# Kernel optimization log

Hardware: AMD Instinct MI355X
Metric: run time of the kernel (lower is better)

Reference implementation:

```python
import jax, jax.numpy as jnp
import numpy as np

NUM_TRAIN = 256  # num_train_anchors
N, A, T = 8, 131072, 64


def _make_boxes(key, shape2):
    # shape2 = (..., 2) of (y, x); returns valid boxes (y1, x1, y2, x2) in [0, 1]
    k1, k2 = jax.random.split(key)
    c1 = jax.random.uniform(k1, shape2, dtype=jnp.float32)
    c2 = jax.random.uniform(k2, shape2, dtype=jnp.float32)
    lo = jnp.minimum(c1, c2)
    hi = jnp.maximum(c1, c2)
    return jnp.stack([lo[..., 0], lo[..., 1], hi[..., 0], hi[..., 1]], axis=-1)


def setup_inputs() -> dict:
    key = jax.random.key(0)
    ka, kt, kp, kn = jax.random.split(key, 4)
    return {
        "anchors": _make_boxes(ka, (N, A, 2)),
        "true_bboxes": _make_boxes(kt, (N, T, 2)),
        "rand_pos": jax.random.uniform(kp, (N, A), dtype=jnp.float32),
        "rand_neg": jax.random.uniform(kn, (N, A), dtype=jnp.float32),
    }


def _bbox_overlap(anchors, gt):
    # anchors [A,4], gt [T,4] -> IoU [A,T]
    ay1, ax1, ay2, ax2 = [anchors[:, i] for i in range(4)]
    gy1, gx1, gy2, gx2 = [gt[:, i] for i in range(4)]
    a_area = (ay2 - ay1) * (ax2 - ax1)                       # [A]
    g_area = (gy2 - gy1) * (gx2 - gx1)                       # [T]
    ih = jnp.clip(jnp.minimum(ay2[:, None], gy2[None, :]) - jnp.maximum(ay1[:, None], gy1[None, :]), 0.0)
    iw = jnp.clip(jnp.minimum(ax2[:, None], gx2[None, :]) - jnp.maximum(ax1[:, None], gx1[None, :]), 0.0)
    inter = ih * iw                                          # [A,T]
    union = a_area[:, None] + g_area[None, :] - inter
    return jnp.where(union > 0, inter / jnp.where(union > 0, union, 1.0), 0.0)


def _rank_of(scores):
    # rank[i] = position of element i in ascending sort of scores
    order = jnp.argsort(scores)
    return jnp.zeros(scores.shape[0], jnp.int32).at[order].set(jnp.arange(scores.shape[0], dtype=jnp.int32))


def _compute_bbox_deltas(anchors, gt):
    # standard (dy, dx, dh, dw) encoding with safe denominators
    ah = anchors[:, 2] - anchors[:, 0]
    aw = anchors[:, 3] - anchors[:, 1]
    acy = anchors[:, 0] + 0.5 * ah
    acx = anchors[:, 1] + 0.5 * aw
    gh = gt[:, 2] - gt[:, 0]
    gw = gt[:, 3] - gt[:, 1]
    gcy = gt[:, 0] + 0.5 * gh
    gcx = gt[:, 1] + 0.5 * gw
    ah_s = jnp.where(ah > 0, ah, 1.0)
    aw_s = jnp.where(aw > 0, aw, 1.0)
    gh_s = jnp.where(gh > 0, gh, 1.0)
    gw_s = jnp.where(gw > 0, gw, 1.0)
    return jnp.stack([(gcy - acy) / ah_s, (gcx - acx) / aw_s,
                      jnp.log(gh_s / ah_s), jnp.log(gw_s / aw_s)], axis=-1)


def _get_targets(anchors, gt, r_pos, r_neg):
    na = anchors.shape[0]
    # strip_out_of_bounds_anchors: zero out anchors falling outside [0,1]^2 (keeps static shape)
    inb = (anchors[:, 0] >= 0) & (anchors[:, 1] >= 0) & (anchors[:, 2] <= 1) & (anchors[:, 3] <= 1)
    anchors = jnp.where(inb[:, None], anchors, 0.0)

    overlaps = _bbox_overlap(anchors, gt)                    # [A,T]

    # --- class assignment ---
    iou_max_val = jnp.max(overlaps, axis=1)                  # [A]
    classes = jnp.full((na,), -1, jnp.int32)
    classes = jnp.where(iou_max_val < 0.3, 0, classes)
    iou_max_anchor = jnp.argmax(overlaps, axis=0)            # [T] best anchor per gt
    pos_anchor = jnp.zeros((na,), jnp.int32).at[iou_max_anchor].set(1)
    classes = jnp.where(pos_anchor > 0, 1, classes)
    classes = jnp.where(iou_max_val >= 0.7, 1, classes)

    # --- subsample positives to NUM_TRAIN//2 (uniform random subset) ---
    pos = classes > 0
    rank_p = _rank_of(jnp.where(pos, r_pos, jnp.inf))
    keep_pos = pos & (rank_p < NUM_TRAIN // 2)
    classes = jnp.where(pos & ~keep_pos, -1, classes)
    n_pos = jnp.sum(keep_pos.astype(jnp.int32))

    # --- subsample negatives to NUM_TRAIN - n_pos ---
    desired_neg = NUM_TRAIN - n_pos
    neg = classes == 0
    rank_n = _rank_of(jnp.where(neg, r_neg, jnp.inf))
    keep_neg = neg & (rank_n < desired_neg)
    classes = jnp.where(neg & ~keep_neg, -1, classes)

    # --- deltas for positive anchors ---
    best_gt = jnp.argmax(overlaps, axis=1)                   # [A]
    deltas = _compute_bbox_deltas(anchors, gt[best_gt])      # [A,4]
    deltas = jnp.where((classes > 0)[:, None], deltas, 0.0)
    return classes, deltas


def reference(anchors, true_bboxes, rand_pos, rand_neg):
    classes, deltas = jax.vmap(_get_targets)(anchors, true_bboxes, rand_pos, rand_neg)
    return classes, deltas
```

## Files before the change

kernel.cpp:

```cpp
#include <hip/hip_runtime.h>
#include <stdint.h>

#define N_B 8
#define A_N 131072
#define T_N 64
#define NUM_TRAIN 256
#define NEG_TAU 0.05f
#define ITEM_CAP 1024
#define APT 4
#define GBLK 128
#define SEG 1024

typedef unsigned long long u64;
typedef unsigned int u32;

__device__ __forceinline__ float iou_one(float ay1, float ax1, float ay2, float ax2,
                                         float a_area, float gy1, float gx1, float gy2,
                                         float gx2, float g_area) {
#pragma clang fp contract(off)
    float ih = fmaxf(fminf(ay2, gy2) - fmaxf(ay1, gy1), 0.0f);
    float iw = fmaxf(fminf(ax2, gx2) - fmaxf(ax1, gx1), 0.0f);
    float inter = ih * iw;
    float uni = (a_area + g_area) - inter;
    return uni > 0.0f ? inter / uni : 0.0f;
}

__global__ void __launch_bounds__(256, 4) k_main(const float4* __restrict__ anchors4,
                                                 const float4* __restrict__ gts4,
                                                 const float* __restrict__ rpos,
                                                 const float* __restrict__ rneg,
                                                 unsigned char* __restrict__ preclass,
                                                 u64* __restrict__ colpart,
                                                 u64* __restrict__ pos_list,
                                                 u64* __restrict__ neg_list,
                                                 int* __restrict__ bcp, int* __restrict__ bcn) {
    __shared__ float4 gbox[T_N];
    __shared__ float gars[T_N];
    __shared__ u64 cmax[T_N];
    __shared__ int lp, ln;
    int n = blockIdx.y, bx = blockIdx.x, tid = threadIdx.x, lane = tid & 63;
    int a0 = bx * SEG + tid;
    size_t nA = (size_t)n * A_N;

    if (tid < T_N) {
        float4 gb = gts4[n * T_N + tid];
        gbox[tid] = gb;
        {
#pragma clang fp contract(off)
            gars[tid] = (gb.z - gb.x) * (gb.w - gb.y);
        }
        cmax[tid] = 0;
    }
    if (tid == 0) { lp = 0; ln = 0; }
    __syncthreads();

    float ay1[APT], ax1[APT], ay2[APT], ax2[APT], aar[APT], vmax[APT];
#pragma unroll
    for (int k = 0; k < APT; k++) {
        float4 ab = anchors4[nA + a0 + k * 256];
        float y1 = ab.x, x1 = ab.y, y2 = ab.z, x2 = ab.w;
        bool inb = (y1 >= 0.f) && (x1 >= 0.f) && (y2 <= 1.f) && (x2 <= 1.f);
        if (!inb) { y1 = x1 = y2 = x2 = 0.f; }
        ay1[k] = y1; ax1[k] = x1; ay2[k] = y2; ax2[k] = x2;
        {
#pragma clang fp contract(off)
            aar[k] = (y2 - y1) * (x2 - x1);
        }
        vmax[k] = 0.f;
    }

#pragma unroll 4
    for (int jj = 0; jj < T_N; jj++) {
        int j = (lane + jj) & (T_N - 1);
        float4 gb = gbox[j];
        float gar = gars[j];
        float vb = iou_one(ay1[0], ax1[0], ay2[0], ax2[0], aar[0], gb.x, gb.y, gb.z, gb.w, gar);
        vmax[0] = fmaxf(vmax[0], vb);
        int kb = 0;
#pragma unroll
        for (int k = 1; k < APT; k++) {
            float v = iou_one(ay1[k], ax1[k], ay2[k], ax2[k], aar[k], gb.x, gb.y, gb.z, gb.w, gar);
            vmax[k] = fmaxf(vmax[k], v);
            if (v > vb) { vb = v; kb = k; }
        }
        u64 pk = ((u64)__float_as_uint(vb) << 32) | (u32)(~(u32)(a0 + (kb << 8)));
        atomicMax(&cmax[j], pk);
    }

    size_t segbase = ((size_t)(n * GBLK + bx)) << 10;
#pragma unroll
    for (int k = 0; k < APT; k++) {
        int a = a0 + k * 256;
        float vm = vmax[k];
        int c0 = (vm < 0.3f) ? 0 : ((vm >= 0.7f) ? 1 : -1);
        preclass[nA + a] = (unsigned char)(signed char)c0;
        if (c0 == 1) {
            int s = atomicAdd(&lp, 1);
            pos_list[segbase + s] = ((u64)__float_as_uint(rpos[nA + a]) << 32) | (u32)a;
        } else if (c0 == 0) {
            float r = rneg[nA + a];
            if (r < NEG_TAU) {
                int s = atomicAdd(&ln, 1);
                neg_list[segbase + s] = ((u64)__float_as_uint(r) << 32) | (u32)a;
            }
        }
    }
    __syncthreads();
    if (tid < T_N) colpart[(size_t)((n << 6) + tid) * GBLK + bx] = cmax[tid];
    if (tid == 0) { bcp[n * GBLK + bx] = lp; bcn[n * GBLK + bx] = ln; }
}

__device__ u64 select_kth2(const u64* lists, const int* scnt,
                           const u64* extras, int ecnt, const u32* exbm,
                           int k, float scale, u64 ovf_all,
                           int* hist, u64* items, int* misc, int* wsum, u64* result) {
    int tid = threadIdx.x, lane = tid & 63, wid = tid >> 6;
    hist[tid] = 0;
    if (tid == 0) { misc[0] = 0; *result = ovf_all; }
    __syncthreads();

    int seg = tid >> 1, half = tid & 1;
    int c = scnt[seg];
    const ulonglong2* b2 = (const ulonglong2*)(lists + ((size_t)seg << 10));
    int nch = (c + 1) >> 1;

    {
        ulonglong2 q;
        if (half < nch) q = b2[half];
        for (int ci = half; ci < nch; ci += 2) {
            ulonglong2 qn;
            if (ci + 2 < nch) qn = b2[ci + 2];
            {
                u64 p = q.x; int a = (int)(u32)p;
                if (!exbm || !((exbm[a >> 5] >> (a & 31)) & 1)) {
                    float v = __uint_as_float((u32)(p >> 32));
                    int bb = (int)(v * scale); bb = bb > 255 ? 255 : bb;
                    atomicAdd(&hist[bb], 1);
                }
            }
            if (2 * ci + 1 < c) {
                u64 p = q.y; int a = (int)(u32)p;
                if (!exbm || !((exbm[a >> 5] >> (a & 31)) & 1)) {
                    float v = __uint_as_float((u32)(p >> 32));
                    int bb = (int)(v * scale); bb = bb > 255 ? 255 : bb;
                    atomicAdd(&hist[bb], 1);
                }
            }
            q = qn;
        }
    }
    for (int i = tid; i < ecnt; i += 256) {
        float v = __uint_as_float((u32)(extras[i] >> 32));
        int bb = (int)(v * scale); bb = bb > 255 ? 255 : bb;
        atomicAdd(&hist[bb], 1);
    }
    __syncthreads();

    int h = hist[tid], v = h;
#pragma unroll
    for (int d = 1; d < 64; d <<= 1) {
        int t = __shfl_up(v, d, 64);
        if (lane >= d) v += t;
    }
    if (lane == 63) wsum[wid] = v;
    __syncthreads();
    int base = 0;
    for (int w = 0; w < wid; w++) base += wsum[w];
    int total = wsum[0] + wsum[1] + wsum[2] + wsum[3];
    int incl = base + v, exc = incl - h;
    if (k >= exc && k < incl) { misc[1] = tid; misc[2] = exc; }
    __syncthreads();
    if (k >= total) return ovf_all;
    int b = misc[1], before = misc[2];

    {
        ulonglong2 q;
        if (half < nch) q = b2[half];
        for (int ci = half; ci < nch; ci += 2) {
            ulonglong2 qn;
            if (ci + 2 < nch) qn = b2[ci + 2];
            {
                u64 p = q.x; int a = (int)(u32)p;
                if (!exbm || !((exbm[a >> 5] >> (a & 31)) & 1)) {
                    float vv = __uint_as_float((u32)(p >> 32));
                    int bn = (int)(vv * scale); bn = bn > 255 ? 255 : bn;
                    if (bn == b) { int ix = atomicAdd(&misc[0], 1); if (ix < ITEM_CAP) items[ix] = p; }
                }
            }
            if (2 * ci + 1 < c) {
                u64 p = q.y; int a = (int)(u32)p;
                if (!exbm || !((exbm[a >> 5] >> (a & 31)) & 1)) {
                    float vv = __uint_as_float((u32)(p >> 32));
                    int bn = (int)(vv * scale); bn = bn > 255 ? 255 : bn;
                    if (bn == b) { int ix = atomicAdd(&misc[0], 1); if (ix < ITEM_CAP) items[ix] = p; }
                }
            }
            q = qn;
        }
    }
    for (int i = tid; i < ecnt; i += 256) {
        u64 p = extras[i];
        float vv = __uint_as_float((u32)(p >> 32));
        int bn = (int)(vv * scale); bn = bn > 255 ? 255 : bn;
        if (bn == b) { int ix = atomicAdd(&misc[0], 1); if (ix < ITEM_CAP) items[ix] = p; }
    }
    __syncthreads();
    int m = misc[0]; m = m < ITEM_CAP ? m : ITEM_CAP;
    int target = k - before;
    for (int i = tid; i < m; i += 256) {
        u64 p = items[i];
        int r = 0;
        for (int j = 0; j < m; j++) r += (items[j] < p);
        if (r == target) *result = p;
    }
    __syncthreads();
    u64 res = *result;
    __syncthreads();
    return res;
}

__global__ void __launch_bounds__(256) k_select(const u64* __restrict__ pos_list,
                                                const u64* __restrict__ neg_list,
                                                const int* __restrict__ bcp,
                                                const int* __restrict__ bcn,
                                                const u64* __restrict__ colpart,
                                                const unsigned char* __restrict__ preclass,
                                                const float* __restrict__ rpos,
                                                int* __restrict__ wnr_g,
                                                u64* __restrict__ cutoff) {
    __shared__ int sbp[GBLK], sbn[GBLK];
    __shared__ u64 cq[256];
    __shared__ int wnrs[T_N];
    __shared__ u64 extras[T_N];
    __shared__ int hist[256];
    __shared__ u64 items[ITEM_CAP];
    __shared__ u32 exbm[A_N / 32];
    __shared__ int misc[4];
    __shared__ u64 result;
    __shared__ int wsum[4];
    __shared__ int shr[9];
    int n = blockIdx.x, tid = threadIdx.x, lane = tid & 63, wid = tid >> 6;

    int pv = tid < GBLK ? bcp[n * GBLK + tid] : 0;
    int nv = tid < GBLK ? bcn[n * GBLK + tid] : 0;
    if (tid < GBLK) { sbp[tid] = pv; sbn[tid] = nv; }
#pragma unroll
    for (int off = 32; off > 0; off >>= 1) {
        pv += __shfl_xor(pv, off, 64);
        nv += __shfl_xor(nv, off, 64);
    }
    if (lane == 0) { shr[wid] = pv; shr[4 + wid] = nv; }

#pragma unroll
    for (int i = 0; i < A_N / 32 / 256; i++) exbm[tid + i * 256] = 0;

    {
        int t = tid >> 2, q = tid & 3;
        const u64* cp = colpart + (size_t)((n << 6) + t) * GBLK + q * 32;
        u64 m = 0;
#pragma unroll 8
        for (int i = 0; i < 32; i++) { u64 x = cp[i]; m = x > m ? x : m; }
        cq[tid] = m;
    }
    __syncthreads();
    if (tid < T_N) {
        u64 m = cq[tid * 4];
        u64 x = cq[tid * 4 + 1]; m = x > m ? x : m;
        x = cq[tid * 4 + 2]; m = x > m ? x : m;
        x = cq[tid * 4 + 3]; m = x > m ? x : m;
        int w = (int)(~(u32)(m & 0xFFFFFFFFull));
        wnrs[tid] = w;
        wnr_g[n * T_N + tid] = w;
        atomicOr(&exbm[w >> 5], 1u << (w & 31));
    }
    __syncthreads();
    if (tid < T_N) {
        int w = wnrs[tid];
        bool dup = false;
        for (int t2 = 0; t2 < tid; t2++) dup |= (wnrs[t2] == w);
        int pc = (int)(signed char)preclass[(size_t)n * A_N + w];
        bool val = !dup && (pc != 1);
        u64 mask = __ballot(val);
        if (val) {
            int ix = (int)__popcll(mask & ((1ull << lane) - 1));
            extras[ix] = ((u64)__float_as_uint(rpos[(size_t)n * A_N + w]) << 32) | (u32)w;
        }
        if (tid == 0) shr[8] = (int)__popcll(mask);
    }
    __syncthreads();
    int extra_cnt = shr[8];
    int P = shr[0] + shr[1] + shr[2] + shr[3] + extra_cnt;

    u64 cpos = select_kth2(pos_list + (((size_t)n * GBLK) << 10), sbp,
                           extras, extra_cnt, nullptr,
                           NUM_TRAIN / 2, 256.0f, ~0ull,
                           hist, items, misc, wsum, &result);
    int n_pos = P < NUM_TRAIN / 2 ? P : NUM_TRAIN / 2;
    int k_neg = NUM_TRAIN - n_pos;
    u64 cneg = select_kth2(neg_list + (((size_t)n * GBLK) << 10), sbn,
                           nullptr, 0, exbm,
                           k_neg, 256.0f / NEG_TAU, ((u64)__float_as_uint(NEG_TAU) << 32),
                           hist, items, misc, wsum, &result);
    if (tid == 0) { cutoff[2 * n] = cpos; cutoff[2 * n + 1] = cneg; }
}

__global__ void __launch_bounds__(256) k_final(const float4* __restrict__ anchors4,
                                               const float4* __restrict__ gts4,
                                               const u32* __restrict__ preclass32,
                                               const int* __restrict__ wnr_g,
                                               const float4* __restrict__ rpos4,
                                               const float4* __restrict__ rneg4,
                                               const u64* __restrict__ cutoff,
                                               float4* __restrict__ out_classes4,
                                               float4* __restrict__ out_deltas) {
    __shared__ float4 gbox[T_N];
    __shared__ float gars[T_N];
    __shared__ u32 wbm[32];
    int n = blockIdx.y, bx = blockIdx.x, tid = threadIdx.x;
    if (tid < 32) wbm[tid] = 0;
    __syncthreads();
    if (tid < T_N) {
        float4 gb = gts4[n * T_N + tid];
        gbox[tid] = gb;
        {
#pragma clang fp contract(off)
            gars[tid] = (gb.z - gb.x) * (gb.w - gb.y);
        }
        int w = wnr_g[n * T_N + tid];
        int d = w - bx * SEG;
        if ((u32)d < (u32)SEG) atomicOr(&wbm[d >> 5], 1u << (d & 31));
    }
    __syncthreads();

    size_t gi4 = ((size_t)n * A_N) / 4 + bx * 256 + tid;
    u32 pcw = preclass32[gi4];
    float4 rp = rpos4[gi4];
    float4 rn = rneg4[gi4];
    float rpv[4] = {rp.x, rp.y, rp.z, rp.w};
    float rnv[4] = {rn.x, rn.y, rn.z, rn.w};
    int a0 = (bx * 256 + tid) * 4;
    u64 cp = cutoff[2 * n], cn = cutoff[2 * n + 1];

    u32 marked = (wbm[tid >> 3] >> ((tid & 7) * 4)) & 0xF;

    float fcv[4];
#pragma unroll
    for (int j = 0; j < 4; j++) {
        int c = (int)(signed char)((pcw >> (8 * j)) & 0xFF);
        if ((marked >> j) & 1) c = 1;
        int a = a0 + j;
        int fc = -1;
        if (c == 1) {
            u64 p = ((u64)__float_as_uint(rpv[j]) << 32) | (u32)a;
            fc = (p < cp) ? 1 : -1;
        } else if (c == 0) {
            u64 p = ((u64)__float_as_uint(rnv[j]) << 32) | (u32)a;
            fc = (p < cn) ? 0 : -1;
        }
        fcv[j] = (float)fc;

        float4 d = make_float4(0.f, 0.f, 0.f, 0.f);
        if (fc == 1) {
            float4 ab = anchors4[(size_t)n * A_N + a];
            float ay1 = ab.x, ax1 = ab.y, ay2 = ab.z, ax2 = ab.w;
            bool inb = (ay1 >= 0.f) && (ax1 >= 0.f) && (ay2 <= 1.f) && (ax2 <= 1.f);
            if (!inb) { ay1 = ax1 = ay2 = ax2 = 0.f; }
            float a_area;
            {
#pragma clang fp contract(off)
                a_area = (ay2 - ay1) * (ax2 - ax1);
            }
            float vm = 0.f; int jb = 0;
            for (int t = 0; t < T_N; t++) {
                float4 gb = gbox[t];
                float v = iou_one(ay1, ax1, ay2, ax2, a_area, gb.x, gb.y, gb.z, gb.w, gars[t]);
                bool g = v > vm;
                vm = g ? v : vm;
                jb = g ? t : jb;
            }
            float4 gb = gbox[jb];
            float ah = ay2 - ay1, aw = ax2 - ax1;
            float acy = ay1 + 0.5f * ah, acx = ax1 + 0.5f * aw;
            float gh = gb.z - gb.x, gw = gb.w - gb.y;
            float gcy = gb.x + 0.5f * gh, gcx = gb.y + 0.5f * gw;
            float ah_s = ah > 0.f ? ah : 1.f, aw_s = aw > 0.f ? aw : 1.f;
            float gh_s = gh > 0.f ? gh : 1.f, gw_s = gw > 0.f ? gw : 1.f;
            d.x = (gcy - acy) / ah_s;
            d.y = (gcx - acx) / aw_s;
            d.z = logf(gh_s / ah_s);
            d.w = logf(gw_s / aw_s);
        }
        out_deltas[(size_t)n * A_N + a] = d;
    }
    out_classes4[gi4] = make_float4(fcv[0], fcv[1], fcv[2], fcv[3]);
}

extern "C" void kernel_launch(void* const* d_in, const int* in_sizes, int n_in,
                              void* d_out, int out_size, void* d_ws, size_t ws_size,
                              hipStream_t stream) {
    const float* anchors = (const float*)d_in[0];
    const float* gts     = (const float*)d_in[1];
    const float* rpos    = (const float*)d_in[2];
    const float* rneg    = (const float*)d_in[3];

    char* p = (char*)d_ws;
    u64* cutoff   = (u64*)p;  p += 2 * N_B * sizeof(u64);
    u64* colpart  = (u64*)p;  p += (size_t)N_B * T_N * GBLK * sizeof(u64);
    u64* pos_list = (u64*)p;  p += (size_t)N_B * GBLK * SEG * sizeof(u64);
    u64* neg_list = (u64*)p;  p += (size_t)N_B * GBLK * SEG * sizeof(u64);
    unsigned char* preclass = (unsigned char*)p; p += (size_t)N_B * A_N;
    int* bcp  = (int*)p;  p += N_B * GBLK * sizeof(int);
    int* bcn  = (int*)p;  p += N_B * GBLK * sizeof(int);
    int* wnr  = (int*)p;  p += N_B * T_N * sizeof(int);

    float* out_classes = (float*)d_out;
    float4* out_deltas = (float4*)(out_classes + (size_t)N_B * A_N);

    k_main<<<dim3(GBLK, N_B), 256, 0, stream>>>(
        (const float4*)anchors, (const float4*)gts, rpos, rneg,
        preclass, colpart, pos_list, neg_list, bcp, bcn);
    k_select<<<N_B, 256, 0, stream>>>(pos_list, neg_list, bcp, bcn, colpart,
                                      preclass, rpos, wnr, cutoff);
    k_final<<<dim3(GBLK, N_B), 256, 0, stream>>>(
        (const float4*)anchors, (const float4*)gts, (const u32*)preclass, wnr,
        (const float4*)rpos, (const float4*)rneg, cutoff,
        (float4*)out_classes, out_deltas);
}
```

Before: 176.4 us.

## Fuse three kernels into one cooperative kernel with grid syncs

Merges the main IoU pass, the selection and the final output pass into one cooperative kernel that separates the phases with grid.sync, and falls back to three launches when co-residency is not possible. The selection phase is split across two blocks per image, one for the positive cutoff and one for the negative cutoff. The large exclusion bitmap in shared memory is replaced by a small open-addressing hash set so the shared union stays small enough for full occupancy. This aims to remove launch gaps and serialized selection time, at the cost of grid-sync overhead and hash probing.

```diff
diff --git a/kernel.cpp b/kernel.cpp
--- a/kernel.cpp
+++ b/kernel.cpp
@@ -1,18 +1,29 @@
 #include <hip/hip_runtime.h>
+#include <hip/hip_cooperative_groups.h>
 #include <stdint.h>
+
+namespace cg = cooperative_groups;
 
 #define N_B 8
 #define A_N 131072
 #define T_N 64
 #define NUM_TRAIN 256
 #define NEG_TAU 0.05f
-#define ITEM_CAP 1024
+#define ITEM_CAP 512
+#define HSET 512
 #define APT 4
 #define GBLK 128
 #define SEG 1024
 
 typedef unsigned long long u64;
 typedef unsigned int u32;
+
+struct SA { float4 gbox[T_N]; float gars[T_N]; u64 cmax[T_N]; int lcnt[2]; };
+struct SB { int sbp[GBLK]; int sbn[GBLK]; u64 cq[256]; int wnrs[T_N]; u64 extras[T_N];
+            int hist[256]; u64 items[ITEM_CAP]; int hset[HSET];
+            int misc[4]; int wsum[4]; int shr[10]; u64 result; };
+struct SC { float4 gbox[T_N]; float gars[T_N]; u32 wbm[32]; };
+union SMem { SA a; SB b; SC c; };
 
 __device__ __forceinline__ float iou_one(float ay1, float ax1, float ay2, float ax2,
                                          float a_area, float gy1, float gx1, float gy2,
@@ -25,33 +36,36 @@
     return uni > 0.0f ? inter / uni : 0.0f;
 }
 
-__global__ void __launch_bounds__(256, 4) k_main(const float4* __restrict__ anchors4,
-                                                 const float4* __restrict__ gts4,
-                                                 const float* __restrict__ rpos,
-                                                 const float* __restrict__ rneg,
-                                                 unsigned char* __restrict__ preclass,
-                                                 u64* __restrict__ colpart,
-                                                 u64* __restrict__ pos_list,
-                                                 u64* __restrict__ neg_list,
-                                                 int* __restrict__ bcp, int* __restrict__ bcn) {
-    __shared__ float4 gbox[T_N];
-    __shared__ float gars[T_N];
-    __shared__ u64 cmax[T_N];
-    __shared__ int lp, ln;
-    int n = blockIdx.y, bx = blockIdx.x, tid = threadIdx.x, lane = tid & 63;
+__device__ __forceinline__ bool in_hset(const int* hset, int a) {
+    u32 h = ((u32)a * 2654435761u) >> 23 & (HSET - 1);
+    while (true) {
+        int v = hset[h];
+        if (v == -1) return false;
+        if (v == a) return true;
+        h = (h + 1) & (HSET - 1);
+    }
+}
+
+__device__ void phaseA(int n, int bx, const float4* __restrict__ anchors4,
+                       const float4* __restrict__ gts4, const float* __restrict__ rpos,
+                       const float* __restrict__ rneg, unsigned char* __restrict__ preclass,
+                       u64* __restrict__ colpart, u64* __restrict__ pos_list,
+                       u64* __restrict__ neg_list, int* __restrict__ bcp,
+                       int* __restrict__ bcn, SA* s) {
+    int tid = threadIdx.x, lane = tid & 63;
     int a0 = bx * SEG + tid;
     size_t nA = (size_t)n * A_N;
 
     if (tid < T_N) {
         float4 gb = gts4[n * T_N + tid];
-        gbox[tid] = gb;
+        s->gbox[tid] = gb;
         {
 #pragma clang fp contract(off)
-            gars[tid] = (gb.z - gb.x) * (gb.w - gb.y);
-        }
-        cmax[tid] = 0;
-    }
-    if (tid == 0) { lp = 0; ln = 0; }
+            s->gars[tid] = (gb.z - gb.x) * (gb.w - gb.y);
+        }
+        s->cmax[tid] = 0;
+    }
+    if (tid < 2) s->lcnt[tid] = 0;
     __syncthreads();
 
     float ay1[APT], ax1[APT], ay2[APT], ax2[APT], aar[APT], vmax[APT];
@@ -72,8 +86,8 @@
 #pragma unroll 4
     for (int jj = 0; jj < T_N; jj++) {
         int j = (lane + jj) & (T_N - 1);
-        float4 gb = gbox[j];
-        float gar = gars[j];
+        float4 gb = s->gbox[j];
+        float gar = s->gars[j];
         float vb = iou_one(ay1[0], ax1[0], ay2[0], ax2[0], aar[0], gb.x, gb.y, gb.z, gb.w, gar);
         vmax[0] = fmaxf(vmax[0], vb);
         int kb = 0;
@@ -84,7 +98,7 @@
             if (v > vb) { vb = v; kb = k; }
         }
         u64 pk = ((u64)__float_as_uint(vb) << 32) | (u32)(~(u32)(a0 + (kb << 8)));
-        atomicMax(&cmax[j], pk);
+        atomicMax(&s->cmax[j], pk);
     }
 
     size_t segbase = ((size_t)(n * GBLK + bx)) << 10;
@@ -95,28 +109,27 @@
         int c0 = (vm < 0.3f) ? 0 : ((vm >= 0.7f) ? 1 : -1);
         preclass[nA + a] = (unsigned char)(signed char)c0;
         if (c0 == 1) {
-            int s = atomicAdd(&lp, 1);
-            pos_list[segbase + s] = ((u64)__float_as_uint(rpos[nA + a]) << 32) | (u32)a;
+            int sl = atomicAdd(&s->lcnt[0], 1);
+            pos_list[segbase + sl] = ((u64)__float_as_uint(rpos[nA + a]) << 32) | (u32)a;
         } else if (c0 == 0) {
             float r = rneg[nA + a];
             if (r < NEG_TAU) {
-                int s = atomicAdd(&ln, 1);
-                neg_list[segbase + s] = ((u64)__float_as_uint(r) << 32) | (u32)a;
-            }
-        }
-    }
-    __syncthreads();
-    if (tid < T_N) colpart[(size_t)((n << 6) + tid) * GBLK + bx] = cmax[tid];
-    if (tid == 0) { bcp[n * GBLK + bx] = lp; bcn[n * GBLK + bx] = ln; }
+                int sl = atomicAdd(&s->lcnt[1], 1);
+                neg_list[segbase + sl] = ((u64)__float_as_uint(r) << 32) | (u32)a;
+            }
+        }
+    }
+    __syncthreads();
+    if (tid < T_N) colpart[(size_t)((n << 6) + tid) * GBLK + bx] = s->cmax[tid];
+    if (tid == 0) { bcp[n * GBLK + bx] = s->lcnt[0]; bcn[n * GBLK + bx] = s->lcnt[1]; }
 }
 
 __device__ u64 select_kth2(const u64* lists, const int* scnt,
-                           const u64* extras, int ecnt, const u32* exbm,
-                           int k, float scale, u64 ovf_all,
-                           int* hist, u64* items, int* misc, int* wsum, u64* result) {
+                           const u64* extras, int ecnt, bool use_excl,
+                           int k, float scale, u64 ovf_all, SB* s) {
     int tid = threadIdx.x, lane = tid & 63, wid = tid >> 6;
-    hist[tid] = 0;
-    if (tid == 0) { misc[0] = 0; *result = ovf_all; }
+    s->hist[tid] = 0;
+    if (tid == 0) { s->misc[0] = 0; s->result = ovf_all; }
     __syncthreads();
 
     int seg = tid >> 1, half = tid & 1;
@@ -132,18 +145,18 @@
             if (ci + 2 < nch) qn = b2[ci + 2];
             {
                 u64 p = q.x; int a = (int)(u32)p;
-                if (!exbm || !((exbm[a >> 5] >> (a & 31)) & 1)) {
+                if (!use_excl || !in_hset(s->hset, a)) {
                     float v = __uint_as_float((u32)(p >> 32));
                     int bb = (int)(v * scale); bb = bb > 255 ? 255 : bb;
-                    atomicAdd(&hist[bb], 1);
+                    atomicAdd(&s->hist[bb], 1);
                 }
             }
             if (2 * ci + 1 < c) {
                 u64 p = q.y; int a = (int)(u32)p;
-                if (!exbm || !((exbm[a >> 5] >> (a & 31)) & 1)) {
+                if (!use_excl || !in_hset(s->hset, a)) {
                     float v = __uint_as_float((u32)(p >> 32));
                     int bb = (int)(v * scale); bb = bb > 255 ? 255 : bb;
-                    atomicAdd(&hist[bb], 1);
+                    atomicAdd(&s->hist[bb], 1);
                 }
             }
             q = qn;
@@ -152,26 +165,26 @@
     for (int i = tid; i < ecnt; i += 256) {
         float v = __uint_as_float((u32)(extras[i] >> 32));
         int bb = (int)(v * scale); bb = bb > 255 ? 255 : bb;
-        atomicAdd(&hist[bb], 1);
-    }
-    __syncthreads();
-
-    int h = hist[tid], v = h;
+        atomicAdd(&s->hist[bb], 1);
+    }
+    __syncthreads();
+
+    int h = s->hist[tid], v = h;
 #pragma unroll
     for (int d = 1; d < 64; d <<= 1) {
         int t = __shfl_up(v, d, 64);
         if (lane >= d) v += t;
     }
-    if (lane == 63) wsum[wid] = v;
+    if (lane == 63) s->wsum[wid] = v;
     __syncthreads();
     int base = 0;
-    for (int w = 0; w < wid; w++) base += wsum[w];
-    int total = wsum[0] + wsum[1] + wsum[2] + wsum[3];
+    for (int w = 0; w < wid; w++) base += s->wsum[w];
+    int total = s->wsum[0] + s->wsum[1] + s->wsum[2] + s->wsum[3];
     int incl = base + v, exc = incl - h;
-    if (k >= exc && k < incl) { misc[1] = tid; misc[2] = exc; }
+    if (k >= exc && k < incl) { s->misc[1] = tid; s->misc[2] = exc; }
     __syncthreads();
     if (k >= total) return ovf_all;
-    int b = misc[1], before = misc[2];
+    int b = s->misc[1], before = s->misc[2];
 
     {
         ulonglong2 q;
@@ -181,18 +194,18 @@
             if (ci + 2 < nch) qn = b2[ci + 2];
             {
                 u64 p = q.x; int a = (int)(u32)p;
-                if (!exbm || !((exbm[a >> 5] >> (a & 31)) & 1)) {
+                if (!use_excl || !in_hset(s->hset, a)) {
                     float vv = __uint_as_float((u32)(p >> 32));
                     int bn = (int)(vv * scale); bn = bn > 255 ? 255 : bn;
-                    if (bn == b) { int ix = atomicAdd(&misc[0], 1); if (ix < ITEM_CAP) items[ix] = p; }
+                    if (bn == b) { int ix = atomicAdd(&s->misc[0], 1); if (ix < ITEM_CAP) s->items[ix] = p; }
                 }
             }
             if (2 * ci + 1 < c) {
                 u64 p = q.y; int a = (int)(u32)p;
-                if (!exbm || !((exbm[a >> 5] >> (a & 31)) & 1)) {
+                if (!use_excl || !in_hset(s->hset, a)) {
                     float vv = __uint_as_float((u32)(p >> 32));
                     int bn = (int)(vv * scale); bn = bn > 255 ? 255 : bn;
-                    if (bn == b) { int ix = atomicAdd(&misc[0], 1); if (ix < ITEM_CAP) items[ix] = p; }
+                    if (bn == b) { int ix = atomicAdd(&s->misc[0], 1); if (ix < ITEM_CAP) s->items[ix] = p; }
                 }
             }
             q = qn;
@@ -202,57 +215,40 @@
         u64 p = extras[i];
         float vv = __uint_as_float((u32)(p >> 32));
         int bn = (int)(vv * scale); bn = bn > 255 ? 255 : bn;
-        if (bn == b) { int ix = atomicAdd(&misc[0], 1); if (ix < ITEM_CAP) items[ix] = p; }
-    }
-    __syncthreads();
-    int m = misc[0]; m = m < ITEM_CAP ? m : ITEM_CAP;
+        if (bn == b) { int ix = atomicAdd(&s->misc[0], 1); if (ix < ITEM_CAP) s->items[ix] = p; }
+    }
+    __syncthreads();
+    int m = s->misc[0]; m = m < ITEM_CAP ? m : ITEM_CAP;
     int target = k - before;
     for (int i = tid; i < m; i += 256) {
-        u64 p = items[i];
+        u64 p = s->items[i];
         int r = 0;
-        for (int j = 0; j < m; j++) r += (items[j] < p);
-        if (r == target) *result = p;
-    }
-    __syncthreads();
-    u64 res = *result;
+        for (int j = 0; j < m; j++) r += (s->items[j] < p);
+        if (r == target) s->result = p;
+    }
+    __syncthreads();
+    u64 res = s->result;
     __syncthreads();
     return res;
 }
 
-__global__ void __launch_bounds__(256) k_select(const u64* __restrict__ pos_list,
-                                                const u64* __restrict__ neg_list,
-                                                const int* __restrict__ bcp,
-                                                const int* __restrict__ bcn,
-                                                const u64* __restrict__ colpart,
-                                                const unsigned char* __restrict__ preclass,
-                                                const float* __restrict__ rpos,
-                                                int* __restrict__ wnr_g,
-                                                u64* __restrict__ cutoff) {
-    __shared__ int sbp[GBLK], sbn[GBLK];
-    __shared__ u64 cq[256];
-    __shared__ int wnrs[T_N];
-    __shared__ u64 extras[T_N];
-    __shared__ int hist[256];
-    __shared__ u64 items[ITEM_CAP];
-    __shared__ u32 exbm[A_N / 32];
-    __shared__ int misc[4];
-    __shared__ u64 result;
-    __shared__ int wsum[4];
-    __shared__ int shr[9];
-    int n = blockIdx.x, tid = threadIdx.x, lane = tid & 63, wid = tid >> 6;
+__device__ void phaseB(int n, int role, const u64* __restrict__ pos_list,
+                       const u64* __restrict__ neg_list, const int* __restrict__ bcp,
+                       const int* __restrict__ bcn, const u64* __restrict__ colpart,
+                       const unsigned char* __restrict__ preclass,
+                       const float* __restrict__ rpos, int* __restrict__ wnr_g,
+                       u64* __restrict__ cutoff, SB* s) {
+    int tid = threadIdx.x, lane = tid & 63, wid = tid >> 6;
+    size_t nA = (size_t)n * A_N;
 
     int pv = tid < GBLK ? bcp[n * GBLK + tid] : 0;
     int nv = tid < GBLK ? bcn[n * GBLK + tid] : 0;
-    if (tid < GBLK) { sbp[tid] = pv; sbn[tid] = nv; }
-#pragma unroll
-    for (int off = 32; off > 0; off >>= 1) {
-        pv += __shfl_xor(pv, off, 64);
-        nv += __shfl_xor(nv, off, 64);
-    }
-    if (lane == 0) { shr[wid] = pv; shr[4 + wid] = nv; }
-
-#pragma unroll
-    for (int i = 0; i < A_N / 32 / 256; i++) exbm[tid + i * 256] = 0;
+    if (tid < GBLK) { s->sbp[tid] = pv; s->sbn[tid] = nv; }
+#pragma unroll
+    for (int off = 32; off > 0; off >>= 1) pv += __shfl_xor(pv, off, 64);
+    if (lane == 0) s->shr[wid] = pv;
+
+    for (int i = tid; i < HSET; i += 256) s->hset[i] = -1;
 
     {
         int t = tid >> 2, q = tid & 3;
@@ -260,79 +256,81 @@
         u64 m = 0;
 #pragma unroll 8
         for (int i = 0; i < 32; i++) { u64 x = cp[i]; m = x > m ? x : m; }
-        cq[tid] = m;
+        s->cq[tid] = m;
     }
     __syncthreads();
     if (tid < T_N) {
-        u64 m = cq[tid * 4];
-        u64 x = cq[tid * 4 + 1]; m = x > m ? x : m;
-        x = cq[tid * 4 + 2]; m = x > m ? x : m;
-        x = cq[tid * 4 + 3]; m = x > m ? x : m;
+        u64 m = s->cq[tid * 4];
+        u64 x = s->cq[tid * 4 + 1]; m = x > m ? x : m;
+        x = s->cq[tid * 4 + 2]; m = x > m ? x : m;
+        x = s->cq[tid * 4 + 3]; m = x > m ? x : m;
         int w = (int)(~(u32)(m & 0xFFFFFFFFull));
-        wnrs[tid] = w;
-        wnr_g[n * T_N + tid] = w;
-        atomicOr(&exbm[w >> 5], 1u << (w & 31));
+        s->wnrs[tid] = w;
+        if (role == 0) wnr_g[n * T_N + tid] = w;
+        u32 hh = ((u32)w * 2654435761u) >> 23 & (HSET - 1);
+        while (true) {
+            int old = atomicCAS(&s->hset[hh], -1, w);
+            if (old == -1 || old == w) break;
+            hh = (hh + 1) & (HSET - 1);
+        }
     }
     __syncthreads();
     if (tid < T_N) {
-        int w = wnrs[tid];
+        int w = s->wnrs[tid];
         bool dup = false;
-        for (int t2 = 0; t2 < tid; t2++) dup |= (wnrs[t2] == w);
-        int pc = (int)(signed char)preclass[(size_t)n * A_N + w];
+        for (int t2 = 0; t2 < tid; t2++) dup |= (s->wnrs[t2] == w);
+        int pc = (int)(signed char)preclass[nA + w];
         bool val = !dup && (pc != 1);
         u64 mask = __ballot(val);
-        if (val) {
+        if (role == 0 && val) {
             int ix = (int)__popcll(mask & ((1ull << lane) - 1));
-            extras[ix] = ((u64)__float_as_uint(rpos[(size_t)n * A_N + w]) << 32) | (u32)w;
-        }
-        if (tid == 0) shr[8] = (int)__popcll(mask);
-    }
-    __syncthreads();
-    int extra_cnt = shr[8];
-    int P = shr[0] + shr[1] + shr[2] + shr[3] + extra_cnt;
-
-    u64 cpos = select_kth2(pos_list + (((size_t)n * GBLK) << 10), sbp,
-                           extras, extra_cnt, nullptr,
-                           NUM_TRAIN / 2, 256.0f, ~0ull,
-                           hist, items, misc, wsum, &result);
-    int n_pos = P < NUM_TRAIN / 2 ? P : NUM_TRAIN / 2;
-    int k_neg = NUM_TRAIN - n_pos;
-    u64 cneg = select_kth2(neg_list + (((size_t)n * GBLK) << 10), sbn,
-                           nullptr, 0, exbm,
-                           k_neg, 256.0f / NEG_TAU, ((u64)__float_as_uint(NEG_TAU) << 32),
-                           hist, items, misc, wsum, &result);
-    if (tid == 0) { cutoff[2 * n] = cpos; cutoff[2 * n + 1] = cneg; }
-}
-
-__global__ void __launch_bounds__(256) k_final(const float4* __restrict__ anchors4,
-                                               const float4* __restrict__ gts4,
-                                               const u32* __restrict__ preclass32,
-                                               const int* __restrict__ wnr_g,
-                                               const float4* __restrict__ rpos4,
-                                               const float4* __restrict__ rneg4,
-                                               const u64* __restrict__ cutoff,
-                                               float4* __restrict__ out_classes4,
-                                               float4* __restrict__ out_deltas) {
-    __shared__ float4 gbox[T_N];
-    __shared__ float gars[T_N];
-    __shared__ u32 wbm[32];
-    int n = blockIdx.y, bx = blockIdx.x, tid = threadIdx.x;
-    if (tid < 32) wbm[tid] = 0;
+            s->extras[ix] = ((u64)__float_as_uint(rpos[nA + w]) << 32) | (u32)w;
+        }
+        if (tid == 0) s->shr[8] = (int)__popcll(mask);
+    }
+    __syncthreads();
+    int extra_cnt = s->shr[8];
+    int P = s->shr[0] + s->shr[1] + s->shr[2] + s->shr[3] + extra_cnt;
+
+    if (role == 0) {
+        u64 cpos = select_kth2(pos_list + (((size_t)n * GBLK) << 10), s->sbp,
+                               s->extras, extra_cnt, false,
+                               NUM_TRAIN / 2, 256.0f, ~0ull, s);
+        if (tid == 0) cutoff[2 * n] = cpos;
+    } else {
+        int n_pos = P < NUM_TRAIN / 2 ? P : NUM_TRAIN / 2;
+        int k_neg = NUM_TRAIN - n_pos;
+        u64 cneg = select_kth2(neg_list + (((size_t)n * GBLK) << 10), s->sbn,
+                               nullptr, 0, true,
+                               k_neg, 256.0f / NEG_TAU, ((u64)__float_as_uint(NEG_TAU) << 32), s);
+        if (tid == 0) cutoff[2 * n + 1] = cneg;
+    }
+}
+
+__device__ void phaseC(int n, int bx, const float4* __restrict__ anchors4,
+                       const float4* __restrict__ gts4, const u32* __restrict__ preclass32,
+                       const int* __restrict__ wnr_g, const float4* __restrict__ rpos4,
+                       const float4* __restrict__ rneg4, const u64* __restrict__ cutoff,
+                       float4* __restrict__ out_classes4, float4* __restrict__ out_deltas,
+                       SC* s) {
+    int tid = threadIdx.x;
+    size_t nA = (size_t)n * A_N;
+    if (tid < 32) s->wbm[tid] = 0;
     __syncthreads();
     if (tid < T_N) {
         float4 gb = gts4[n * T_N + tid];
-        gbox[tid] = gb;
+        s->gbox[tid] = gb;
         {
 #pragma clang fp contract(off)
-            gars[tid] = (gb.z - gb.x) * (gb.w - gb.y);
+            s->gars[tid] = (gb.z - gb.x) * (gb.w - gb.y);
         }
         int w = wnr_g[n * T_N + tid];
         int d = w - bx * SEG;
-        if ((u32)d < (u32)SEG) atomicOr(&wbm[d >> 5], 1u << (d & 31));
-    }
-    __syncthreads();
-
-    size_t gi4 = ((size_t)n * A_N) / 4 + bx * 256 + tid;
+        if ((u32)d < (u32)SEG) atomicOr(&s->wbm[d >> 5], 1u << (d & 31));
+    }
+    __syncthreads();
+
+    size_t gi4 = nA / 4 + bx * 256 + tid;
     u32 pcw = preclass32[gi4];
     float4 rp = rpos4[gi4];
     float4 rn = rneg4[gi4];
@@ -341,7 +339,7 @@
     int a0 = (bx * 256 + tid) * 4;
     u64 cp = cutoff[2 * n], cn = cutoff[2 * n + 1];
 
-    u32 marked = (wbm[tid >> 3] >> ((tid & 7) * 4)) & 0xF;
+    u32 marked = (s->wbm[tid >> 3] >> ((tid & 7) * 4)) & 0xF;
 
     float fcv[4];
 #pragma unroll
@@ -361,7 +359,7 @@
 
         float4 d = make_float4(0.f, 0.f, 0.f, 0.f);
         if (fc == 1) {
-            float4 ab = anchors4[(size_t)n * A_N + a];
+            float4 ab = anchors4[nA + a];
             float ay1 = ab.x, ax1 = ab.y, ay2 = ab.z, ax2 = ab.w;
             bool inb = (ay1 >= 0.f) && (ax1 >= 0.f) && (ay2 <= 1.f) && (ax2 <= 1.f);
             if (!inb) { ay1 = ax1 = ay2 = ax2 = 0.f; }
@@ -372,13 +370,13 @@
             }
             float vm = 0.f; int jb = 0;
             for (int t = 0; t < T_N; t++) {
-                float4 gb = gbox[t];
-                float v = iou_one(ay1, ax1, ay2, ax2, a_area, gb.x, gb.y, gb.z, gb.w, gars[t]);
+                float4 gb = s->gbox[t];
+                float v = iou_one(ay1, ax1, ay2, ax2, a_area, gb.x, gb.y, gb.z, gb.w, s->gars[t]);
                 bool g = v > vm;
                 vm = g ? v : vm;
                 jb = g ? t : jb;
             }
-            float4 gb = gbox[jb];
+            float4 gb = s->gbox[jb];
             float ah = ay2 - ay1, aw = ax2 - ax1;
             float acy = ay1 + 0.5f * ah, acx = ax1 + 0.5f * aw;
             float gh = gb.z - gb.x, gw = gb.w - gb.y;
@@ -390,18 +388,71 @@
             d.z = logf(gh_s / ah_s);
             d.w = logf(gw_s / aw_s);
         }
-        out_deltas[(size_t)n * A_N + a] = d;
+        out_deltas[nA + a] = d;
     }
     out_classes4[gi4] = make_float4(fcv[0], fcv[1], fcv[2], fcv[3]);
+}
+
+__global__ void __launch_bounds__(256, 4) k_fused(
+    const float4* __restrict__ anchors4, const float4* __restrict__ gts4,
+    const float* __restrict__ rpos, const float* __restrict__ rneg,
+    unsigned char* __restrict__ preclass, u64* __restrict__ colpart,
+    u64* __restrict__ pos_list, u64* __restrict__ neg_list,
+    int* __restrict__ bcp, int* __restrict__ bcn,
+    int* __restrict__ wnr_g, u64* __restrict__ cutoff,
+    float4* __restrict__ out_classes4, float4* __restrict__ out_deltas) {
+    __shared__ SMem s;
+    cg::grid_group grid = cg::this_grid();
+    int n = blockIdx.y, bx = blockIdx.x;
+    phaseA(n, bx, anchors4, gts4, rpos, rneg, preclass, colpart, pos_list, neg_list,
+           bcp, bcn, &s.a);
+    grid.sync();
+    if (bx < 2) phaseB(n, bx, pos_list, neg_list, bcp, bcn, colpart, preclass, rpos,
+                       wnr_g, cutoff, &s.b);
+    grid.sync();
+    phaseC(n, bx, anchors4, gts4, (const u32*)preclass, wnr_g,
+           (const float4*)rpos, (const float4*)rneg, cutoff, out_classes4, out_deltas, &s.c);
+}
+
+__global__ void __launch_bounds__(256, 4) k_A(
+    const float4* __restrict__ anchors4, const float4* __restrict__ gts4,
+    const float* __restrict__ rpos, const float* __restrict__ rneg,
+    unsigned char* __restrict__ preclass, u64* __restrict__ colpart,
+    u64* __restrict__ pos_list, u64* __restrict__ neg_list,
+    int* __restrict__ bcp, int* __restrict__ bcn) {
+    __shared__ SMem s;
+    phaseA(blockIdx.y, blockIdx.x, anchors4, gts4, rpos, rneg, preclass, colpart,
+           pos_list, neg_list, bcp, bcn, &s.a);
+}
+
+__global__ void __launch_bounds__(256) k_B(
+    const u64* __restrict__ pos_list, const u64* __restrict__ neg_list,
+    const int* __restrict__ bcp, const int* __restrict__ bcn,
+    const u64* __restrict__ colpart, const unsigned char* __restrict__ preclass,
+    const float* __restrict__ rpos, int* __restrict__ wnr_g, u64* __restrict__ cutoff) {
+    __shared__ SMem s;
+    phaseB(blockIdx.y, blockIdx.x, pos_list, neg_list, bcp, bcn, colpart, preclass,
+           rpos, wnr_g, cutoff, &s.b);
+}
+
+__global__ void __launch_bounds__(256, 4) k_C(
+    const float4* __restrict__ anchors4, const float4* __restrict__ gts4,
+    const u32* __restrict__ preclass32, const int* __restrict__ wnr_g,
+    const float4* __restrict__ rpos4, const float4* __restrict__ rneg4,
+    const u64* __restrict__ cutoff, float4* __restrict__ out_classes4,
+    float4* __restrict__ out_deltas) {
+    __shared__ SMem s;
+    phaseC(blockIdx.y, blockIdx.x, anchors4, gts4, preclass32, wnr_g, rpos4, rneg4,
+           cutoff, out_classes4, out_deltas, &s.c);
 }
 
 extern "C" void kernel_launch(void* const* d_in, const int* in_sizes, int n_in,
                               void* d_out, int out_size, void* d_ws, size_t ws_size,
                               hipStream_t stream) {
-    const float* anchors = (const float*)d_in[0];
-    const float* gts     = (const float*)d_in[1];
-    const float* rpos    = (const float*)d_in[2];
-    const float* rneg    = (const float*)d_in[3];
+    const float4* anchors4 = (const float4*)d_in[0];
+    const float4* gts4     = (const float4*)d_in[1];
+    const float*  rpos     = (const float*)d_in[2];
+    const float*  rneg     = (const float*)d_in[3];
 
     char* p = (char*)d_ws;
     u64* cutoff   = (u64*)p;  p += 2 * N_B * sizeof(u64);
@@ -413,16 +464,36 @@
     int* bcn  = (int*)p;  p += N_B * GBLK * sizeof(int);
     int* wnr  = (int*)p;  p += N_B * T_N * sizeof(int);
 
-    float* out_classes = (float*)d_out;
-    float4* out_deltas = (float4*)(out_classes + (size_t)N_B * A_N);
-
-    k_main<<<dim3(GBLK, N_B), 256, 0, stream>>>(
-        (const float4*)anchors, (const float4*)gts, rpos, rneg,
-        preclass, colpart, pos_list, neg_list, bcp, bcn);
-    k_select<<<N_B, 256, 0, stream>>>(pos_list, neg_list, bcp, bcn, colpart,
-                                      preclass, rpos, wnr, cutoff);
-    k_final<<<dim3(GBLK, N_B), 256, 0, stream>>>(
-        (const float4*)anchors, (const float4*)gts, (const u32*)preclass, wnr,
-        (const float4*)rpos, (const float4*)rneg, cutoff,
-        (float4*)out_classes, out_deltas);
-}
+    float4* out_classes4 = (float4*)d_out;
+    float4* out_deltas   = (float4*)((float*)d_out + (size_t)N_B * A_N);
+
+    int maxB = 0, numCU = 0, dev = 0;
+    hipGetDevice(&dev);
+    hipDeviceGetAttribute(&numCU, hipDeviceAttributeMultiprocessorCount, dev);
+    hipError_t oe = hipOccupancyMaxActiveBlocksPerMultiprocessor(&maxB, (const void*)k_fused,
+                                                                 256, 0);
+    bool coop = (oe == hipSuccess) && numCU > 0 &&
+                ((long)maxB * (long)numCU >= (long)GBLK * N_B);
+
+    if (coop) {
+        void* kargs[] = {
+            (void*)&anchors4, (void*)&gts4, (void*)&rpos, (void*)&rneg,
+            (void*)&preclass, (void*)&colpart, (void*)&pos_list, (void*)&neg_list,
+            (void*)&bcp, (void*)&bcn, (void*)&wnr, (void*)&cutoff,
+            (void*)&out_classes4, (void*)&out_deltas
+        };
+        hipError_t le = hipLaunchCooperativeKernel((const void*)k_fused,
+                                                   dim3(GBLK, N_B), dim3(256),
+                                                   kargs, 0, stream);
+        if (le != hipSuccess) coop = false;
+    }
+    if (!coop) {
+        k_A<<<dim3(GBLK, N_B), 256, 0, stream>>>(anchors4, gts4, rpos, rneg, preclass,
+                                                 colpart, pos_list, neg_list, bcp, bcn);
+        k_B<<<dim3(2, N_B), 256, 0, stream>>>(pos_list, neg_list, bcp, bcn, colpart,
+                                              preclass, rpos, wnr, cutoff);
+        k_C<<<dim3(GBLK, N_B), 256, 0, stream>>>(anchors4, gts4, (const u32*)preclass, wnr,
+                                                 (const float4*)rpos, (const float4*)rneg,
+                                                 cutoff, out_classes4, out_deltas);
+    }
+}
```

New measurement: 177.4 us. No clear change (+0.5%).
